# Kernel optimization log

Hardware: AMD Instinct MI355X
Metric: run time of the kernel (lower is better)

## Reference

```python
import jax, jax.numpy as jnp
import numpy as np

B, L, D, H = 8, 1024, 512, 8
EPS = 1e-5

def setup_inputs() -> dict:
    key = jax.random.key(0)
    ks = jax.random.split(key, 12)
    s = lambda fan_in: 1.0 / np.sqrt(fan_in)
    u = lambda k, shape, sc: jax.random.uniform(k, shape, jnp.float32, -sc, sc)
    return {
        "input": jax.random.normal(ks[0], (B, L, D), jnp.float32),
        "wq": u(ks[1], (D, H * D), s(D)), "bq": u(ks[2], (H * D,), s(D)),
        "wk": u(ks[3], (D, H * D), s(D)), "bk": u(ks[4], (H * D,), s(D)),
        "wv": u(ks[5], (D, H * D), s(D)), "bv": u(ks[6], (H * D,), s(D)),
        "score_w": u(ks[7], (2 * D, 1), s(2 * D)), "score_b": u(ks[8], (1,), s(2 * D)),
        "fc_w": u(ks[9], (H * D, D), s(H * D)), "fc_b": u(ks[10], (D,), s(H * D)),
        "ln_g": jnp.ones((D,), jnp.float32), "ln_b": jnp.zeros((D,), jnp.float32),
    }

def reference(input, wq, bq, wk, bk, wv, bv, score_w, score_b, fc_w, fc_b, ln_g, ln_b):
    x = input
    b, l, d = x.shape
    h = wq.shape[1] // d
    # project and fold heads into leading batch dim: (h*b, l, d)
    def proj(w, bias):
        y = (x @ w + bias).reshape(b, l, h, d)
        return y.transpose(2, 0, 1, 3).reshape(h * b, l, d)
    q = proj(wq, bq)
    k = proj(wk, bk)
    v = proj(wv, bv)
    # _score(cat(k_i, q_j)) decomposed: k part uses score_w[:d], q part score_w[d:]
    sk = (k @ score_w[:d])[:, :, 0]   # (h*b, l) -> row index i
    sq = (q @ score_w[d:])[:, :, 0]   # (h*b, l) -> col index j
    kq = jnp.tanh(sk[:, :, None] + sq[:, None, :] + score_b[0])  # (h*b, l, l)
    # faithful to original bug: softmax over trailing size-1 dim -> all ones
    score = jax.nn.softmax(kq[..., None], axis=-1)[..., 0]       # (h*b, l, l)
    out = jnp.einsum('nij,njd->nid', score, v)                   # (h*b, l, d)
    out = out.reshape(h, b, l, d).transpose(1, 2, 0, 3).reshape(b, l, h * d)
    out = out @ fc_w + fc_b
    y = out + x
    mu = jnp.mean(y, axis=-1, keepdims=True)
    var = jnp.var(y, axis=-1, keepdims=True)
    return (y - mu) / jnp.sqrt(var + EPS) * ln_g + ln_b
```

## Files before the change

### kernel.cpp

```cpp
#include <hip/hip_runtime.h>

#define BB 8
#define LL 1024
#define DD 512
#define HDIM 4096
#define EPS_LN 1e-5f
#define NB 256
#define NT 1024
#define POISON_I ((int)0xAAAAAAAAu)


__device__ __forceinline__ void grid_bar(int* base, int g, int my) {
    __syncthreads();
    if (threadIdx.x == 0) {
        asm volatile("" ::: "memory");
        __builtin_amdgcn_s_waitcnt(0);
        int v = __hip_atomic_fetch_add(base + (1 + g) * 32, 1,
                                       __ATOMIC_RELAXED,
                                       __HIP_MEMORY_SCOPE_AGENT);
        bool released = false;
        if (v == POISON_I + 31) {
            int m = __hip_atomic_fetch_add(base, 1, __ATOMIC_RELAXED,
                                           __HIP_MEMORY_SCOPE_AGENT);
            if (m == POISON_I + 7) {
                __builtin_amdgcn_fence(__ATOMIC_RELEASE, "agent");
#pragma unroll
                for (int r = 0; r < 8; ++r)
                    __hip_atomic_store(base + (9 + r) * 32, 1,
                                       __ATOMIC_RELAXED,
                                       __HIP_MEMORY_SCOPE_AGENT);
                released = true;
            }
        }
        if (!released) {
            int* f = base + (9 + my) * 32;
            while (__hip_atomic_load(f, __ATOMIC_RELAXED,
                                     __HIP_MEMORY_SCOPE_AGENT) != 1)
                __builtin_amdgcn_s_sleep(2);
        }
        asm volatile("" ::: "memory");
    }
    __syncthreads();
}

__global__ __launch_bounds__(NT) void mha_fused(
    const float* __restrict__ x,
    const float* __restrict__ wv,
    const float* __restrict__ bv,
    const float* __restrict__ fcw,
    const float* __restrict__ fcb,
    const float* __restrict__ g,
    const float* __restrict__ beta,
    float* __restrict__ out,
    float* __restrict__ xs,
    float* __restrict__ u_part,
    int* __restrict__ bar)
{
    __shared__ float redA[16][DD];
    __shared__ float xs_lds[BB * DD];
    __shared__ float Tpart[32][BB * 32];
    __shared__ float T_lds[BB * 32];
    __shared__ float red2[2][DD];
    __shared__ float uf[DD];

    const int tid = threadIdx.x;
    const int bi  = blockIdx.x;
    const int b   = bi >> 5;
    const int gB  = bi >> 5;
    const int my  = bi & 7;

    const int dv   = tid & 63;
    const int rowg = tid >> 6;
    float4 xa0, xa1, xb0, xb1;

    {
        const float* basep = x + ((size_t)(bi * 32 + rowg * 2)) * DD + dv * 8;
        xa0 = *(const float4*)(basep);
        xa1 = *(const float4*)(basep + 4);
        xb0 = *(const float4*)(basep + DD);
        xb1 = *(const float4*)(basep + DD + 4);

        float4* dst = (float4*)&redA[rowg][dv * 8];
        dst[0] = make_float4(xa0.x + xb0.x, xa0.y + xb0.y,
                             xa0.z + xb0.z, xa0.w + xb0.w);
        dst[1] = make_float4(xa1.x + xb1.x, xa1.y + xb1.y,
                             xa1.z + xb1.z, xa1.w + xb1.w);
        __syncthreads();

        if (tid < DD) {
            float s = 0.f;
#pragma unroll
            for (int gg = 0; gg < 16; ++gg) s += redA[gg][tid];
            atomicAdd(&xs[b * DD + tid], s);
        }
    }

    grid_bar(bar, gB, my);

    {
        ((float4*)xs_lds)[tid] = ((const float4*)xs)[tid];
        __syncthreads();

        const int chunk = bi >> 1;
        const int half  = bi & 1;
        const int c0 = chunk * 32;
        const int c  = tid & 31;
        const int kg = tid >> 5;
        float acc[BB];
#pragma unroll
        for (int bb = 0; bb < BB; ++bb) acc[bb] = 0.f;

        const float* wp = wv + c0 + c;
        const float4* xsv = (const float4*)xs_lds;
#pragma unroll
        for (int k4 = kg * 4; k4 < kg * 4 + 4; ++k4) {
            const int k = k4 * 4;
            float w0 = wp[(size_t)(k + 0) * HDIM];
            float w1 = wp[(size_t)(k + 1) * HDIM];
            float w2 = wp[(size_t)(k + 2) * HDIM];
            float w3 = wp[(size_t)(k + 3) * HDIM];
#pragma unroll
            for (int bb = 0; bb < BB; ++bb) {
                float4 xv = xsv[bb * 128 + k4];
                acc[bb] += xv.x * w0 + xv.y * w1 + xv.z * w2 + xv.w * w3;
            }
        }
#pragma unroll
        for (int bb = 0; bb < BB; ++bb) Tpart[kg][bb * 32 + c] = acc[bb];
        __syncthreads();

        if (tid < BB * 32) {
            float s = 0.f;
#pragma unroll
            for (int gg = 0; gg < 32; ++gg) s += Tpart[gg][tid];
            s += 1024.f * bv[c0 + (tid & 31)];
            T_lds[tid] = s;
        }
        __syncthreads();

        const int dcol = tid & 255;
        const int cg   = tid >> 8;
        const int bb0  = cg * 2;
        const int dd   = half * 256 + dcol;
        float accu0 = 0.f, accu1 = 0.f;

        const float* fp = fcw + dd;
        for (int cc = 0; cc < 32; ++cc) {
            float f = fp[(size_t)(c0 + cc) * DD];
            accu0 += T_lds[bb0 * 32 + cc] * f;
            accu1 += T_lds[(bb0 + 1) * 32 + cc] * f;
        }
        __hip_atomic_store(&u_part[((size_t)bb0 * 128 + chunk) * DD + dd],
                           accu0, __ATOMIC_RELAXED, __HIP_MEMORY_SCOPE_AGENT);
        __hip_atomic_store(&u_part[((size_t)(bb0 + 1) * 128 + chunk) * DD + dd],
                           accu1, __ATOMIC_RELAXED, __HIP_MEMORY_SCOPE_AGENT);
    }

    grid_bar(bar + 1024, gB, my);

    {
        const int ddv = tid & 511;
        const int kh  = tid >> 9;
        float s = 0.f;
        const float* up = u_part + ((size_t)b * 128 + kh * 64) * DD + ddv;
#pragma unroll 8
        for (int k = 0; k < 64; ++k) s += up[(size_t)k * DD];
        red2[kh][ddv] = s;
        __syncthreads();
        if (tid < DD) uf[tid] = red2[0][tid] + red2[1][tid] + fcb[tid];
        __syncthreads();

        const int lane = dv;
        float4 uq0 = *(const float4*)(uf + lane * 8);
        float4 uq1 = *(const float4*)(uf + lane * 8 + 4);
        float4 g0 = *(const float4*)(g + lane * 8);
        float4 g1 = *(const float4*)(g + lane * 8 + 4);
        float4 b0 = *(const float4*)(beta + lane * 8);
        float4 b1 = *(const float4*)(beta + lane * 8 + 4);

#pragma unroll
        for (int it = 0; it < 2; ++it) {
            const int row = bi * 32 + rowg * 2 + it;
            const size_t off = (size_t)row * DD + lane * 8;
            float4 x0 = (it == 0) ? xa0 : xb0;
            float4 x1 = (it == 0) ? xa1 : xb1;

            float y[8];
            y[0] = x0.x + uq0.x;  y[1] = x0.y + uq0.y;
            y[2] = x0.z + uq0.z;  y[3] = x0.w + uq0.w;
            y[4] = x1.x + uq1.x;  y[5] = x1.y + uq1.y;
            y[6] = x1.z + uq1.z;  y[7] = x1.w + uq1.w;

            float s1 = 0.f, ss = 0.f;
#pragma unroll
            for (int i = 0; i < 8; ++i) { s1 += y[i]; ss += y[i] * y[i]; }
#pragma unroll
            for (int m = 1; m < 64; m <<= 1) {
                s1 += __shfl_xor(s1, m, 64);
                ss += __shfl_xor(ss, m, 64);
            }
            const float mean = s1 * (1.f / 512.f);
            const float var  = ss * (1.f / 512.f) - mean * mean;
            const float rstd = rsqrtf(var + EPS_LN);

            float4 o0, o1;
            o0.x = (y[0] - mean) * rstd * g0.x + b0.x;
            o0.y = (y[1] - mean) * rstd * g0.y + b0.y;
            o0.z = (y[2] - mean) * rstd * g0.z + b0.z;
            o0.w = (y[3] - mean) * rstd * g0.w + b0.w;
            o1.x = (y[4] - mean) * rstd * g1.x + b1.x;
            o1.y = (y[5] - mean) * rstd * g1.y + b1.y;
            o1.z = (y[6] - mean) * rstd * g1.z + b1.z;
            o1.w = (y[7] - mean) * rstd * g1.w + b1.w;
            *(float4*)(out + off)     = o0;
            *(float4*)(out + off + 4) = o1;
        }
    }
}

extern "C" void kernel_launch(void* const* d_in, const int* in_sizes, int n_in,
                              void* d_out, int out_size, void* d_ws, size_t ws_size,
                              hipStream_t stream) {
    const float* x   = (const float*)d_in[0];
    const float* wv  = (const float*)d_in[5];
    const float* bv  = (const float*)d_in[6];
    const float* fcw = (const float*)d_in[9];
    const float* fcb = (const float*)d_in[10];
    const float* lng = (const float*)d_in[11];
    const float* lnb = (const float*)d_in[12];

    float* xs     = (float*)d_ws;
    int*   bar    = (int*)((char*)d_ws + 16 * 1024);
    float* u_part = (float*)((char*)d_ws + 32 * 1024);
    float* out = (float*)d_out;

    mha_fused<<<NB, NT, 0, stream>>>(x, wv, bv, fcw, fcb, lng, lnb,
                                     out, xs, u_part, bar);
}
```

Before: 118.6 us.

## Prefetch weights before grid barrier and reduce fc output with atomics

Each block now owns a 16-column slice of the value projection. It loads its wv and fc_w slices into registers before the first grid barrier, so those global loads overlap the barrier wait. The partial fc outputs are summed with atomicAdd into a small per-batch buffer, replacing the 128-way partial buffer and its strided reduction after the second barrier. The barrier spin-sleep is also shortened. In exchange there is atomic contention on 4096 addresses, higher register pressure, and reliance on the workspace's initial contents for the atomic accumulation.

```diff
diff --git a/kernel.cpp b/kernel.cpp
--- a/kernel.cpp
+++ b/kernel.cpp
@@ -11,10 +11,9 @@
 
 
 __device__ __forceinline__ void grid_bar(int* base, int g, int my) {
+    asm volatile("s_waitcnt vmcnt(0)" ::: "memory");
     __syncthreads();
     if (threadIdx.x == 0) {
-        asm volatile("" ::: "memory");
-        __builtin_amdgcn_s_waitcnt(0);
         int v = __hip_atomic_fetch_add(base + (1 + g) * 32, 1,
                                        __ATOMIC_RELAXED,
                                        __HIP_MEMORY_SCOPE_AGENT);
@@ -36,7 +35,7 @@
             int* f = base + (9 + my) * 32;
             while (__hip_atomic_load(f, __ATOMIC_RELAXED,
                                      __HIP_MEMORY_SCOPE_AGENT) != 1)
-                __builtin_amdgcn_s_sleep(2);
+                __builtin_amdgcn_s_sleep(1);
         }
         asm volatile("" ::: "memory");
     }
@@ -53,14 +52,14 @@
     const float* __restrict__ beta,
     float* __restrict__ out,
     float* __restrict__ xs,
-    float* __restrict__ u_part,
+    float* __restrict__ u,
     int* __restrict__ bar)
 {
     __shared__ float redA[16][DD];
     __shared__ float xs_lds[BB * DD];
-    __shared__ float Tpart[32][BB * 32];
-    __shared__ float T_lds[BB * 32];
-    __shared__ float red2[2][DD];
+    __shared__ float Tpart[64][144];
+    __shared__ float Tpart2[8][144];
+    __shared__ float T_lds[BB * 16];
     __shared__ float uf[DD];
 
     const int tid = threadIdx.x;
@@ -95,79 +94,77 @@
         }
     }
 
+    const int chunk = ((bi & 7) << 5) | (bi >> 3);
+    const int c0  = chunk * 16;
+    const int cB  = tid & 15;
+    const int kg  = tid >> 4;
+    const int ddB = tid & 511;
+    const int bh  = tid >> 9;
+
+    float wvp[8];
+#pragma unroll
+    for (int j = 0; j < 8; ++j)
+        wvp[j] = wv[(size_t)(kg * 8 + j) * HDIM + c0 + cB];
+    float fcp[16];
+#pragma unroll
+    for (int cc = 0; cc < 16; ++cc)
+        fcp[cc] = fcw[(size_t)(c0 + cc) * DD + ddB];
+
     grid_bar(bar, gB, my);
 
     {
         ((float4*)xs_lds)[tid] = ((const float4*)xs)[tid];
         __syncthreads();
 
-        const int chunk = bi >> 1;
-        const int half  = bi & 1;
-        const int c0 = chunk * 32;
-        const int c  = tid & 31;
-        const int kg = tid >> 5;
         float acc[BB];
 #pragma unroll
         for (int bb = 0; bb < BB; ++bb) acc[bb] = 0.f;
-
-        const float* wp = wv + c0 + c;
-        const float4* xsv = (const float4*)xs_lds;
-#pragma unroll
-        for (int k4 = kg * 4; k4 < kg * 4 + 4; ++k4) {
-            const int k = k4 * 4;
-            float w0 = wp[(size_t)(k + 0) * HDIM];
-            float w1 = wp[(size_t)(k + 1) * HDIM];
-            float w2 = wp[(size_t)(k + 2) * HDIM];
-            float w3 = wp[(size_t)(k + 3) * HDIM];
-#pragma unroll
-            for (int bb = 0; bb < BB; ++bb) {
-                float4 xv = xsv[bb * 128 + k4];
-                acc[bb] += xv.x * w0 + xv.y * w1 + xv.z * w2 + xv.w * w3;
-            }
-        }
-#pragma unroll
-        for (int bb = 0; bb < BB; ++bb) Tpart[kg][bb * 32 + c] = acc[bb];
-        __syncthreads();
-
-        if (tid < BB * 32) {
+#pragma unroll
+        for (int j = 0; j < 8; ++j) {
+            const int k = kg * 8 + j;
+#pragma unroll
+            for (int bb = 0; bb < BB; ++bb)
+                acc[bb] += xs_lds[bb * DD + k] * wvp[j];
+        }
+#pragma unroll
+        for (int bb = 0; bb < BB; ++bb) Tpart[kg][bb * 16 + cB] = acc[bb];
+        __syncthreads();
+
+        {
+            const int e   = tid & 127;
+            const int sub = tid >> 7;
             float s = 0.f;
 #pragma unroll
-            for (int gg = 0; gg < 32; ++gg) s += Tpart[gg][tid];
-            s += 1024.f * bv[c0 + (tid & 31)];
+            for (int q = 0; q < 8; ++q) s += Tpart[sub * 8 + q][e];
+            Tpart2[sub][e] = s;
+        }
+        __syncthreads();
+        if (tid < BB * 16) {
+            float s = 0.f;
+#pragma unroll
+            for (int q = 0; q < 8; ++q) s += Tpart2[q][tid];
+            s += 1024.f * bv[c0 + (tid & 15)];
             T_lds[tid] = s;
         }
         __syncthreads();
 
-        const int dcol = tid & 255;
-        const int cg   = tid >> 8;
-        const int bb0  = cg * 2;
-        const int dd   = half * 256 + dcol;
-        float accu0 = 0.f, accu1 = 0.f;
-
-        const float* fp = fcw + dd;
-        for (int cc = 0; cc < 32; ++cc) {
-            float f = fp[(size_t)(c0 + cc) * DD];
-            accu0 += T_lds[bb0 * 32 + cc] * f;
-            accu1 += T_lds[(bb0 + 1) * 32 + cc] * f;
-        }
-        __hip_atomic_store(&u_part[((size_t)bb0 * 128 + chunk) * DD + dd],
-                           accu0, __ATOMIC_RELAXED, __HIP_MEMORY_SCOPE_AGENT);
-        __hip_atomic_store(&u_part[((size_t)(bb0 + 1) * 128 + chunk) * DD + dd],
-                           accu1, __ATOMIC_RELAXED, __HIP_MEMORY_SCOPE_AGENT);
+        float accu[4] = {0.f, 0.f, 0.f, 0.f};
+#pragma unroll
+        for (int cc = 0; cc < 16; ++cc) {
+            float f = fcp[cc];
+#pragma unroll
+            for (int q = 0; q < 4; ++q)
+                accu[q] += T_lds[(bh * 4 + q) * 16 + cc] * f;
+        }
+#pragma unroll
+        for (int q = 0; q < 4; ++q)
+            atomicAdd(&u[(bh * 4 + q) * DD + ddB], accu[q]);
     }
 
     grid_bar(bar + 1024, gB, my);
 
     {
-        const int ddv = tid & 511;
-        const int kh  = tid >> 9;
-        float s = 0.f;
-        const float* up = u_part + ((size_t)b * 128 + kh * 64) * DD + ddv;
-#pragma unroll 8
-        for (int k = 0; k < 64; ++k) s += up[(size_t)k * DD];
-        red2[kh][ddv] = s;
-        __syncthreads();
-        if (tid < DD) uf[tid] = red2[0][tid] + red2[1][tid] + fcb[tid];
+        if (tid < DD) uf[tid] = u[b * DD + tid] + fcb[tid];
         __syncthreads();
 
         const int lane = dv;
@@ -229,11 +226,11 @@
     const float* lng = (const float*)d_in[11];
     const float* lnb = (const float*)d_in[12];
 
-    float* xs     = (float*)d_ws;
-    int*   bar    = (int*)((char*)d_ws + 16 * 1024);
-    float* u_part = (float*)((char*)d_ws + 32 * 1024);
+    float* xs  = (float*)d_ws;
+    int*   bar = (int*)((char*)d_ws + 16 * 1024);
+    float* u   = (float*)((char*)d_ws + 32 * 1024);
     float* out = (float*)d_out;
 
     mha_fused<<<NB, NT, 0, stream>>>(x, wv, bv, fcw, fcb, lng, lnb,
-                                     out, xs, u_part, bar);
+                                     out, xs, u, bar);
 }
```

Result: slower. 121.5 us (+2.5%).
